# Kernel tuning notes

Measured on AMD Instinct MI355X. Metric: run time of the kernel, lower is better.

The kernel has to match this reference:

```python
import jax, jax.numpy as jnp
from jax import lax
import numpy as np

ALPHA, BETA, DECAY, GAMMA = 0.9, 0.1, 0.9, 0.5
KW = 5  # temporal_window


def setup_inputs() -> dict:
    key = jax.random.key(0)
    k1, k2 = jax.random.split(key)
    B, T, F = 128, 128, 2048
    x = jax.random.normal(k1, (B, T, F), dtype=jnp.float32)
    init_threshold = jnp.array(1.0, dtype=jnp.float32)
    conv_w = jax.random.normal(k2, (1, 1, KW), dtype=jnp.float32) * 0.2  # Conv1d(1,1,KW) weight
    conv_b = jnp.zeros((1,), dtype=jnp.float32)
    spatial_attn = jnp.array([1.0], dtype=jnp.float32)
    return {"x": x, "init_threshold": init_threshold, "conv_w": conv_w,
            "conv_b": conv_b, "spatial_attn": spatial_attn}


def _forward(x, init_threshold, conv_w, conv_b, spatial_attn):
    B, T, F = x.shape
    # --- temporal encoding: Conv1d(1,1,KW,'same') along time, per (batch,feature) ---
    xt = jnp.transpose(x, (0, 2, 1)).reshape(B * F, 1, T)  # [B*F,1,T]
    conv = lax.conv_general_dilated(xt, conv_w, window_strides=(1,), padding='SAME',
                                    dimension_numbers=('NCH', 'OIH', 'NCH'))
    conv = conv + conv_b[None, :, None]
    x = jnp.transpose(conv.reshape(B, F, T), (0, 2, 1))  # [B,T,F]
    # --- spatial attention ---
    w = jax.nn.sigmoid(spatial_attn * x.mean(axis=1, keepdims=True))  # [B,1,F]
    x = x * (1.0 + GAMMA * w)
    # --- LIF recurrence over time ---
    mem0 = jnp.zeros((B, F), dtype=x.dtype)
    thr0 = jnp.broadcast_to(init_threshold, (B, F)).astype(x.dtype)
    hist0 = jnp.zeros((B, 3, F), dtype=x.dtype)
    pi = jnp.float32(np.pi)

    def step(carry, xt):
        mem, thr, hist = carry
        mem = DECAY * mem + xt
        spike = 0.5 * (jnp.arctan(pi * (mem - thr) / 2) / pi + 0.5)  # multi_atan surrogate
        hist = jnp.concatenate([hist[:, 1:], spike[:, None]], axis=1)  # [B,3,F]
        avg = hist.mean(axis=1)  # [B,F]
        new_thr = ALPHA * thr + (1.0 - ALPHA) * init_threshold + BETA * avg
        mem = mem - spike * lax.stop_gradient(new_thr)
        return (mem, new_thr, hist), spike

    (mem, _, _), spikes = lax.scan(step, (mem0, thr0, hist0), jnp.transpose(x, (1, 0, 2)))
    return jnp.transpose(spikes, (1, 0, 2)), mem  # [B,T,F], [B,F]


def reference(x, init_threshold, conv_w, conv_b, spatial_attn):
    return _forward(x, init_threshold, conv_w, conv_b, spatial_attn)
```

## Files before the change

### kernel.cpp

```cpp
#include <hip/hip_runtime.h>
#include <math.h>

constexpr int B = 128, T = 128, F = 2048, KW = 5;
#define ALPHA 0.9f
#define BETA  0.1f
#define DECAY 0.9f
#define GAMMA 0.5f

typedef float v2f __attribute__((ext_vector_type(2)));

__device__ __forceinline__ float atan_fast(float z) {
    float az  = __builtin_fabsf(z);
    float inv = __builtin_amdgcn_rcpf(az);
    bool  big = az > 1.0f;
    float u   = big ? inv : az;
    float u2  = u * u;
    float p   = fmaf(u2, -0.01172120f, 0.05265332f);
    p = fmaf(u2, p, -0.11643287f);
    p = fmaf(u2, p,  0.19354346f);
    p = fmaf(u2, p, -0.33262347f);
    p = fmaf(u2, p,  0.99997726f);
    float r = u * p;
    r = big ? (1.57079632679f - r) : r;
    return copysignf(r, z);
}

__global__ __launch_bounds__(256) void lif_fused_kernel(
    const float* __restrict__ x,
    const float* __restrict__ thr0p,
    const float* __restrict__ convw,
    const float* __restrict__ convb,
    const float* __restrict__ sattn,
    float* __restrict__ out)
{
    const int raw    = blockIdx.x;
    const int xcd    = raw & 7;
    const int slot   = raw >> 3;
    const int b      = xcd * 16 + (slot >> 2);
    const int fchunk = slot & 3;
    const int f      = fchunk * 512 + (int)threadIdx.x * 2;

    const float w0 = convw[0], w1 = convw[1], w2 = convw[2],
                w3 = convw[3], w4 = convw[4];
    const float cb   = convb[0];
    const float thr0 = thr0p[0];
    const float sa   = sattn[0];

    const float* xp = x + (size_t)b * T * F + f;

    v2f s0 = {0.f,0.f}, s1 = {0.f,0.f}, s2 = {0.f,0.f}, s3 = {0.f,0.f},
        s4 = {0.f,0.f}, s5 = {0.f,0.f}, s6 = {0.f,0.f}, s7 = {0.f,0.f};
#pragma unroll 2
    for (int t = 0; t < T; t += 8) {
        v2f v0 = *(const v2f*)(xp + (size_t)(t + 0) * F);
        v2f v1 = *(const v2f*)(xp + (size_t)(t + 1) * F);
        v2f v2 = *(const v2f*)(xp + (size_t)(t + 2) * F);
        v2f v3 = *(const v2f*)(xp + (size_t)(t + 3) * F);
        v2f v4 = *(const v2f*)(xp + (size_t)(t + 4) * F);
        v2f v5 = *(const v2f*)(xp + (size_t)(t + 5) * F);
        v2f v6 = *(const v2f*)(xp + (size_t)(t + 6) * F);
        v2f v7 = *(const v2f*)(xp + (size_t)(t + 7) * F);
        s0 += v0; s1 += v1; s2 += v2; s3 += v3;
        s4 += v4; s5 += v5; s6 += v6; s7 += v7;
    }
    v2f sx = ((s0 + s1) + (s2 + s3)) + ((s4 + s5) + (s6 + s7));

    v2f e0  = *(const v2f*)(xp);
    v2f e1  = *(const v2f*)(xp + (size_t)F);
    v2f em2 = *(const v2f*)(xp + (size_t)(T - 2) * F);
    v2f em1 = *(const v2f*)(xp + (size_t)(T - 1) * F);

    const float W = ((w0 + w1) + (w2 + w3)) + w4;
    v2f csum;
    csum.x = fmaf(W, sx.x, (float)T * cb)
           - (w3 + w4) * e0.x - w4 * e1.x - w0 * em2.x - (w0 + w1) * em1.x;
    csum.y = fmaf(W, sx.y, (float)T * cb)
           - (w3 + w4) * e0.y - w4 * e1.y - w0 * em2.y - (w0 + w1) * em1.y;

    v2f scale;
    {
        float zx = sa * (csum.x * (1.0f / (float)T));
        float zy = sa * (csum.y * (1.0f / (float)T));
        scale.x = 1.0f + GAMMA * (1.0f / (1.0f + expf(-zx)));
        scale.y = 1.0f + GAMMA * (1.0f / (1.0f + expf(-zy)));
    }

    const float PIH    = 1.57079632679f;
    const float INV2PI = 0.15915494309f;
    const float thc    = (1.0f - ALPHA) * thr0;

    v2f mem = {0.f, 0.f};
    v2f thr = {thr0, thr0};
    v2f h1 = {0.f, 0.f}, h2 = {0.f, 0.f};
    v2f a = {0.f, 0.f}, bb = {0.f, 0.f}, c = e0, d = e1;

    float* sp = out + (size_t)b * T * F + f;
    float* mp = out + (size_t)B * T * F + (size_t)b * F + f;

    auto lif_step = [&](int t, v2f e) {
        float cx = fmaf(w0, a.x, fmaf(w1, bb.x, fmaf(w2, c.x,
                   fmaf(w3, d.x, fmaf(w4, e.x, cb)))));
        float cy = fmaf(w0, a.y, fmaf(w1, bb.y, fmaf(w2, c.y,
                   fmaf(w3, d.y, fmaf(w4, e.y, cb)))));
        mem.x = fmaf(DECAY, mem.x, cx * scale.x);
        mem.y = fmaf(DECAY, mem.y, cy * scale.y);
        float spx = fmaf(atan_fast(PIH * (mem.x - thr.x)), INV2PI, 0.25f);
        float spy = fmaf(atan_fast(PIH * (mem.y - thr.y)), INV2PI, 0.25f);
        float avx = (h1.x + h2.x + spx) * (1.0f / 3.0f);
        float avy = (h1.y + h2.y + spy) * (1.0f / 3.0f);
        h1 = h2; h2.x = spx; h2.y = spy;
        thr.x = fmaf(ALPHA, thr.x, fmaf(BETA, avx, thc));
        thr.y = fmaf(ALPHA, thr.y, fmaf(BETA, avy, thc));
        mem.x = fmaf(-spx, thr.x, mem.x);
        mem.y = fmaf(-spy, thr.y, mem.y);
        v2f spv = {spx, spy};
        *(v2f*)(sp + (size_t)t * F) = spv;
        a = bb; bb = c; c = d; d = e;
    };

#pragma unroll 8
    for (int t = 0; t < T - 2; ++t) {
        v2f e = *(const v2f*)(xp + (size_t)(t + 2) * F);
        lif_step(t, e);
    }
    lif_step(T - 2, (v2f){0.f, 0.f});
    lif_step(T - 1, (v2f){0.f, 0.f});

    *(v2f*)mp = mem;
}

extern "C" void kernel_launch(void* const* d_in, const int* in_sizes, int n_in,
                              void* d_out, int out_size, void* d_ws, size_t ws_size,
                              hipStream_t stream) {
    const float* x     = (const float*)d_in[0];
    const float* thr0  = (const float*)d_in[1];
    const float* convw = (const float*)d_in[2];
    const float* convb = (const float*)d_in[3];
    const float* sattn = (const float*)d_in[4];
    float* out = (float*)d_out;

    const int total = B * F / 2;
    const int block = 256;
    const int grid  = total / block;

    lif_fused_kernel<<<grid, block, 0, stream>>>(x, thr0, convw, convb, sattn, out);
}
```

Baseline: 255.6 us.

## Process four features per thread with 16-byte accesses and nontemporal stores

Widens each thread's work from two to four adjacent features, so loads and stores become 128-bit and half as many threads are launched. Spike and membrane outputs use nontemporal stores to avoid polluting the cache. The XCD-aware block-to-batch remapping is replaced by a linear mapping, and launch bounds allow more registers per thread. The trade-off is far fewer waves per CU, which reduces latency hiding for the long serial recurrence.

```diff
diff --git a/kernel.cpp b/kernel.cpp
--- a/kernel.cpp
+++ b/kernel.cpp
@@ -7,7 +7,7 @@
 #define DECAY 0.9f
 #define GAMMA 0.5f
 
-typedef float v2f __attribute__((ext_vector_type(2)));
+typedef float v4f __attribute__((ext_vector_type(4)));
 
 __device__ __forceinline__ float atan_fast(float z) {
     float az  = __builtin_fabsf(z);
@@ -25,7 +25,7 @@
     return copysignf(r, z);
 }
 
-__global__ __launch_bounds__(256) void lif_fused_kernel(
+__global__ __launch_bounds__(256, 1) void lif_fused_kernel(
     const float* __restrict__ x,
     const float* __restrict__ thr0p,
     const float* __restrict__ convw,
@@ -33,12 +33,10 @@
     const float* __restrict__ sattn,
     float* __restrict__ out)
 {
-    const int raw    = blockIdx.x;
-    const int xcd    = raw & 7;
-    const int slot   = raw >> 3;
-    const int b      = xcd * 16 + (slot >> 2);
-    const int fchunk = slot & 3;
-    const int f      = fchunk * 512 + (int)threadIdx.x * 2;
+    const int tid   = blockIdx.x * blockDim.x + threadIdx.x;
+    const int fquad = tid & (F / 4 - 1);
+    const int b     = tid >> 9;
+    const int f     = fquad * 4;
 
     const float w0 = convw[0], w1 = convw[1], w2 = convw[2],
                 w3 = convw[3], w4 = convw[4];
@@ -48,85 +46,75 @@
 
     const float* xp = x + (size_t)b * T * F + f;
 
-    v2f s0 = {0.f,0.f}, s1 = {0.f,0.f}, s2 = {0.f,0.f}, s3 = {0.f,0.f},
-        s4 = {0.f,0.f}, s5 = {0.f,0.f}, s6 = {0.f,0.f}, s7 = {0.f,0.f};
+    v4f s0 = 0.f, s1 = 0.f, s2 = 0.f, s3 = 0.f,
+        s4 = 0.f, s5 = 0.f, s6 = 0.f, s7 = 0.f;
 #pragma unroll 2
     for (int t = 0; t < T; t += 8) {
-        v2f v0 = *(const v2f*)(xp + (size_t)(t + 0) * F);
-        v2f v1 = *(const v2f*)(xp + (size_t)(t + 1) * F);
-        v2f v2 = *(const v2f*)(xp + (size_t)(t + 2) * F);
-        v2f v3 = *(const v2f*)(xp + (size_t)(t + 3) * F);
-        v2f v4 = *(const v2f*)(xp + (size_t)(t + 4) * F);
-        v2f v5 = *(const v2f*)(xp + (size_t)(t + 5) * F);
-        v2f v6 = *(const v2f*)(xp + (size_t)(t + 6) * F);
-        v2f v7 = *(const v2f*)(xp + (size_t)(t + 7) * F);
+        v4f v0 = *(const v4f*)(xp + (size_t)(t + 0) * F);
+        v4f v1 = *(const v4f*)(xp + (size_t)(t + 1) * F);
+        v4f v2 = *(const v4f*)(xp + (size_t)(t + 2) * F);
+        v4f v3 = *(const v4f*)(xp + (size_t)(t + 3) * F);
+        v4f v4 = *(const v4f*)(xp + (size_t)(t + 4) * F);
+        v4f v5 = *(const v4f*)(xp + (size_t)(t + 5) * F);
+        v4f v6 = *(const v4f*)(xp + (size_t)(t + 6) * F);
+        v4f v7 = *(const v4f*)(xp + (size_t)(t + 7) * F);
         s0 += v0; s1 += v1; s2 += v2; s3 += v3;
         s4 += v4; s5 += v5; s6 += v6; s7 += v7;
     }
-    v2f sx = ((s0 + s1) + (s2 + s3)) + ((s4 + s5) + (s6 + s7));
+    v4f sx = ((s0 + s1) + (s2 + s3)) + ((s4 + s5) + (s6 + s7));
 
-    v2f e0  = *(const v2f*)(xp);
-    v2f e1  = *(const v2f*)(xp + (size_t)F);
-    v2f em2 = *(const v2f*)(xp + (size_t)(T - 2) * F);
-    v2f em1 = *(const v2f*)(xp + (size_t)(T - 1) * F);
+    v4f e0  = *(const v4f*)(xp);
+    v4f e1  = *(const v4f*)(xp + (size_t)F);
+    v4f em2 = *(const v4f*)(xp + (size_t)(T - 2) * F);
+    v4f em1 = *(const v4f*)(xp + (size_t)(T - 1) * F);
 
     const float W = ((w0 + w1) + (w2 + w3)) + w4;
-    v2f csum;
-    csum.x = fmaf(W, sx.x, (float)T * cb)
-           - (w3 + w4) * e0.x - w4 * e1.x - w0 * em2.x - (w0 + w1) * em1.x;
-    csum.y = fmaf(W, sx.y, (float)T * cb)
-           - (w3 + w4) * e0.y - w4 * e1.y - w0 * em2.y - (w0 + w1) * em1.y;
+    v4f csum = W * sx + (float)T * cb
+             - (w3 + w4) * e0 - w4 * e1 - w0 * em2 - (w0 + w1) * em1;
 
-    v2f scale;
-    {
-        float zx = sa * (csum.x * (1.0f / (float)T));
-        float zy = sa * (csum.y * (1.0f / (float)T));
-        scale.x = 1.0f + GAMMA * (1.0f / (1.0f + expf(-zx)));
-        scale.y = 1.0f + GAMMA * (1.0f / (1.0f + expf(-zy)));
+    v4f scale;
+#pragma unroll
+    for (int j = 0; j < 4; ++j) {
+        float z = sa * (csum[j] * (1.0f / (float)T));
+        scale[j] = 1.0f + GAMMA * (1.0f / (1.0f + expf(-z)));
     }
 
     const float PIH    = 1.57079632679f;
     const float INV2PI = 0.15915494309f;
     const float thc    = (1.0f - ALPHA) * thr0;
 
-    v2f mem = {0.f, 0.f};
-    v2f thr = {thr0, thr0};
-    v2f h1 = {0.f, 0.f}, h2 = {0.f, 0.f};
-    v2f a = {0.f, 0.f}, bb = {0.f, 0.f}, c = e0, d = e1;
+    v4f mem = 0.f;
+    v4f thr = thr0;
+    v4f h1 = 0.f, h2 = 0.f;
+    v4f a = 0.f, bb = 0.f, c = e0, d = e1;
 
     float* sp = out + (size_t)b * T * F + f;
     float* mp = out + (size_t)B * T * F + (size_t)b * F + f;
 
-    auto lif_step = [&](int t, v2f e) {
-        float cx = fmaf(w0, a.x, fmaf(w1, bb.x, fmaf(w2, c.x,
-                   fmaf(w3, d.x, fmaf(w4, e.x, cb)))));
-        float cy = fmaf(w0, a.y, fmaf(w1, bb.y, fmaf(w2, c.y,
-                   fmaf(w3, d.y, fmaf(w4, e.y, cb)))));
-        mem.x = fmaf(DECAY, mem.x, cx * scale.x);
-        mem.y = fmaf(DECAY, mem.y, cy * scale.y);
-        float spx = fmaf(atan_fast(PIH * (mem.x - thr.x)), INV2PI, 0.25f);
-        float spy = fmaf(atan_fast(PIH * (mem.y - thr.y)), INV2PI, 0.25f);
-        float avx = (h1.x + h2.x + spx) * (1.0f / 3.0f);
-        float avy = (h1.y + h2.y + spy) * (1.0f / 3.0f);
-        h1 = h2; h2.x = spx; h2.y = spy;
-        thr.x = fmaf(ALPHA, thr.x, fmaf(BETA, avx, thc));
-        thr.y = fmaf(ALPHA, thr.y, fmaf(BETA, avy, thc));
-        mem.x = fmaf(-spx, thr.x, mem.x);
-        mem.y = fmaf(-spy, thr.y, mem.y);
-        v2f spv = {spx, spy};
-        *(v2f*)(sp + (size_t)t * F) = spv;
+    auto lif_step = [&](int t, v4f e) {
+        v4f ct = w0 * a + w1 * bb + w2 * c + w3 * d + w4 * e + cb;
+        mem = DECAY * mem + ct * scale;
+        v4f spike;
+#pragma unroll
+        for (int j = 0; j < 4; ++j)
+            spike[j] = fmaf(atan_fast(PIH * (mem[j] - thr[j])), INV2PI, 0.25f);
+        v4f avg = (h1 + h2 + spike) * (1.0f / 3.0f);
+        h1 = h2; h2 = spike;
+        thr = ALPHA * thr + (BETA * avg + thc);
+        mem = mem - spike * thr;
+        __builtin_nontemporal_store(spike, (v4f*)(sp + (size_t)t * F));
         a = bb; bb = c; c = d; d = e;
     };
 
 #pragma unroll 8
     for (int t = 0; t < T - 2; ++t) {
-        v2f e = *(const v2f*)(xp + (size_t)(t + 2) * F);
+        v4f e = *(const v4f*)(xp + (size_t)(t + 2) * F);
         lif_step(t, e);
     }
-    lif_step(T - 2, (v2f){0.f, 0.f});
-    lif_step(T - 1, (v2f){0.f, 0.f});
+    lif_step(T - 2, (v4f)0.f);
+    lif_step(T - 1, (v4f)0.f);
 
-    *(v2f*)mp = mem;
+    __builtin_nontemporal_store(mem, (v4f*)mp);
 }
 
 extern "C" void kernel_launch(void* const* d_in, const int* in_sizes, int n_in,
@@ -139,7 +127,7 @@
     const float* sattn = (const float*)d_in[4];
     float* out = (float*)d_out;
 
-    const int total = B * F / 2;
+    const int total = B * F / 4;
     const int block = 256;
     const int grid  = total / block;
 
```

Result: no change. 253.5 us (-0.8%).
